# Kernel optimization log

Measured on AMD Instinct MI355X. Metric: run time of the kernel, lower is better.

## Reference

```python
import jax, jax.numpy as jnp
import numpy as np
from jax import lax

C = 64        # channels / number of Phi heads
HID = 8       # Phi hidden size
FEAT = 2 * 8 * 8  # flattened size after conv+pool
EPS = 1e-5
NEG_SLOPE = 0.01


def setup_inputs() -> dict:
    key = jax.random.key(0)
    ks = jax.random.split(key, 12)
    B = 2048
    x1 = jax.random.normal(ks[0], (B, C, 19, 19), dtype=jnp.float32)
    x2 = jax.random.normal(ks[1], (B, C, 19, 19), dtype=jnp.float32)
    s = 0.1
    conv_w = jax.random.normal(ks[2], (C, 2, 2, 3, 3), dtype=jnp.float32) * s
    conv_b = jax.random.normal(ks[3], (C, 2), dtype=jnp.float32) * s
    bn_g = jnp.ones((C, 2), dtype=jnp.float32)
    bn_b = jnp.zeros((C, 2), dtype=jnp.float32)
    fc1_w = jax.random.normal(ks[4], (C, HID, FEAT), dtype=jnp.float32) * s
    fc1_b = jax.random.normal(ks[5], (C, HID), dtype=jnp.float32) * s
    fc2_w = jax.random.normal(ks[6], (C, 1, HID), dtype=jnp.float32) * s
    fc2_b = jax.random.normal(ks[7], (C, 1), dtype=jnp.float32) * s
    w_out = jax.random.normal(ks[8], (1, C), dtype=jnp.float32) * s
    b_out = jax.random.normal(ks[9], (1,), dtype=jnp.float32) * s
    return {
        "x1": x1, "x2": x2,
        "conv_w": conv_w, "conv_b": conv_b,
        "bn_g": bn_g, "bn_b": bn_b,
        "fc1_w": fc1_w, "fc1_b": fc1_b,
        "fc2_w": fc2_w, "fc2_b": fc2_b,
        "w_out": w_out, "b_out": b_out,
    }


def _phi(x, cw, cb, g, b, w1, b1, w2, b2):
    # x: [B,2,19,19], cw: [2,2,3,3]
    y = lax.conv_general_dilated(x, cw, (1, 1), 'VALID',
                                 dimension_numbers=('NCHW', 'OIHW', 'NCHW'))
    y = y + cb[None, :, None, None]                       # [B,2,17,17]
    # BatchNorm2d in training mode: biased batch stats over (N,H,W)
    mean = jnp.mean(y, axis=(0, 2, 3), keepdims=True)
    var = jnp.mean((y - mean) ** 2, axis=(0, 2, 3), keepdims=True)
    y = (y - mean) * lax.rsqrt(var + EPS)
    y = y * g[None, :, None, None] + b[None, :, None, None]
    # LeakyReLU (default slope 0.01)
    y = jnp.where(y > 0, y, NEG_SLOPE * y)
    # MaxPool2d(2): 17x17 -> 8x8 (floor)
    y = lax.reduce_window(y, -jnp.inf, lax.max,
                          (1, 1, 2, 2), (1, 1, 2, 2), 'VALID')
    y = y.reshape(y.shape[0], -1)                         # [B,128]
    y = y @ w1.T + b1                                     # [B,HID]
    y = y @ w2.T + b2                                     # [B,1]
    return y


def reference(x1, x2, conv_w, conv_b, bn_g, bn_b, fc1_w, fc1_b, fc2_w, fc2_b,
              w_out, b_out):
    B = x1.shape[0]
    # per-channel pair input: [C, B, 2, H, W]
    xin = jnp.stack([x1, x2], axis=2).transpose(1, 0, 2, 3, 4)
    outs = jax.vmap(_phi)(xin, conv_w, conv_b, bn_g, bn_b,
                          fc1_w, fc1_b, fc2_w, fc2_b)      # [C, B, 1]
    feat = outs[..., 0].T                                  # [B, C]
    logits = feat @ w_out.T + b_out                        # [B, 1]
    return jax.nn.sigmoid(logits)
```

## Files before the change

kernel.cpp:

```cpp
#include <hip/hip_runtime.h>
#include <math.h>

#define CC    64
#define BATCH 2048
#define EPS   1e-5f
#define SLOPE 0.01f

#define WS_SUMR  0
#define WS_SQR   4096
#define WS_A     8192
#define WS_B     8320
#define WS_WF    8448
#define WS_WB    16640
#define WS_LOGIT 16704
#define WS_POOL  18944
#define WS_NEEDED_BYTES ((size_t)(WS_POOL + (size_t)BATCH * CC * 128) * 4)

__device__ inline unsigned bf16rne(float x) {
    unsigned u = __float_as_uint(x);
    return (u + 0x7fffu + ((u >> 16) & 1u)) >> 16;
}

__device__ inline void pkfma(float2& acc, float2 a, float2 b) {
    asm("v_pk_fma_f32 %0, %1, %2, %0" : "+v"(acc) : "v"(a), "v"(b));
}

template<bool STORE>
__global__ __launch_bounds__(64, 4) void pass1_kernel(
    const float* __restrict__ x1, const float* __restrict__ x2,
    const float* __restrict__ conv_w, const float* __restrict__ conv_b,
    float* __restrict__ ws)
{
    __shared__ __align__(16) float lds[2][760];

    int blk = blockIdx.x;
    int b  = blk >> 5;
    int c0 = (blk & 31) * 2;
    int t  = threadIdx.x;

    const float2* g1 = (const float2*)(x1 + ((size_t)b * 64 + c0) * 361);
    const float2* g2 = (const float2*)(x2 + ((size_t)b * 64 + c0) * 361);
    #pragma unroll
    for (int sl = 0; sl < 6; sl++) {
        int g = t + 64 * sl;
        if (sl < 5 || g < 361) {
            float2 v1 = g1[g];
            float2 v2 = g2[g];
            unsigned e  = 2u * g;
            unsigned r0 = (e * 110377u) >> 21;
            unsigned r1 = ((e + 1u) * 110377u) >> 21;
            int i0 = e + r0;
            int i1 = e + 1 + r1;
            lds[0][i0] = v1.x; lds[0][i1] = v1.y;
            lds[1][i0] = v2.x; lds[1][i1] = v2.y;
        }
    }

    int img = t >> 5;
    int u   = t & 31;
    int o   = u >> 4;
    int p   = u & 15;
    int pi  = p >> 1;
    int pjp = p & 1;
    int c   = c0 + img;

    const float2* wp2 = (const float2*)(conv_w + (size_t)(c * 2 + o) * 18);
    float2 wgt[18];
    #pragma unroll
    for (int j = 0; j < 9; j++) {
        float2 pr = wp2[j];
        wgt[2 * j]     = make_float2(pr.x, pr.x);
        wgt[2 * j + 1] = make_float2(pr.y, pr.y);
    }
    float cbv = conv_b[c * 2 + o];

    __syncthreads();

    float2 A[2][4];
    #pragma unroll
    for (int di = 0; di < 2; di++)
        #pragma unroll
        for (int k = 0; k < 4; k++)
            A[di][k] = make_float2(cbv, cbv);

    int wb = img * 380 + pi * 40 + pjp * 8;

    #pragma unroll
    for (int ic = 0; ic < 2; ic++) {
        const float* plane = &lds[ic][wb];
        const float2* wic = &wgt[ic * 9];
        #pragma unroll
        for (int r = 0; r < 4; r++) {
            const float* row = plane + 20 * r;
            float4 a4 = *(const float4*)(row);
            float4 b4 = *(const float4*)(row + 4);
            float2 c2 = *(const float2*)(row + 8);
            float2 P[9];
            P[0] = make_float2(a4.x, a4.y);
            P[1] = make_float2(a4.y, a4.z);
            P[2] = make_float2(a4.z, a4.w);
            P[3] = make_float2(a4.w, b4.x);
            P[4] = make_float2(b4.x, b4.y);
            P[5] = make_float2(b4.y, b4.z);
            P[6] = make_float2(b4.z, b4.w);
            P[7] = make_float2(b4.w, c2.x);
            P[8] = make_float2(c2.x, c2.y);
            #pragma unroll
            for (int di = 0; di < 2; di++) {
                int ki = r - di;
                if (ki < 0 || ki > 2) continue;
                #pragma unroll
                for (int k = 0; k < 4; k++)
                    #pragma unroll
                    for (int kj = 0; kj < 3; kj++)
                        pkfma(A[di][k], P[2 * k + kj], wic[3 * ki + kj]);
            }
        }
    }

    const float2 one2 = make_float2(1.f, 1.f);
    float2 sp = make_float2(0.f, 0.f), q2 = make_float2(0.f, 0.f);
    #pragma unroll
    for (int di = 0; di < 2; di++)
        #pragma unroll
        for (int k = 0; k < 4; k++) {
            pkfma(sp, A[di][k], one2);
            pkfma(q2, A[di][k], A[di][k]);
        }
    float s = sp.x + sp.y;
    float q = q2.x + q2.y;

    if (STORE) {
        unsigned pk[4];
        #pragma unroll
        for (int k = 0; k < 4; k++) {
            float mx = fmaxf(fmaxf(A[0][k].x, A[0][k].y), fmaxf(A[1][k].x, A[1][k].y));
            float mn = fminf(fminf(A[0][k].x, A[0][k].y), fminf(A[1][k].x, A[1][k].y));
            pk[k] = (bf16rne(mx) << 16) | bf16rne(mn);
        }
        uint4* pool4 = (uint4*)(ws + WS_POOL);
        pool4[((size_t)(b * 64 + c)) * 32 + o * 16 + pi * 2 + pjp] =
            make_uint4(pk[0], pk[1], pk[2], pk[3]);
    }

    int ibase = img * 380;
    #pragma unroll
    for (int rep = 0; rep < 2; rep++) {
        int bidx = p + 16 * rep;
        int bi = bidx < 17 ? 16 : bidx - 17;
        int bj = bidx < 17 ? bidx : 16;
        int bw = ibase + 20 * bi + bj;
        float accb = cbv;
        #pragma unroll
        for (int ic = 0; ic < 2; ic++)
            #pragma unroll
            for (int ki = 0; ki < 3; ki++)
                #pragma unroll
                for (int kj = 0; kj < 3; kj++)
                    accb = fmaf(lds[ic][bw + 20 * ki + kj], wgt[ic * 9 + ki * 3 + kj].x, accb);
        s += accb; q = fmaf(accb, accb, q);
    }
    if (p == 0) {
        int bw = ibase + 20 * 15 + 16;
        float accb = cbv;
        #pragma unroll
        for (int ic = 0; ic < 2; ic++)
            #pragma unroll
            for (int ki = 0; ki < 3; ki++)
                #pragma unroll
                for (int kj = 0; kj < 3; kj++)
                    accb = fmaf(lds[ic][bw + 20 * ki + kj], wgt[ic * 9 + ki * 3 + kj].x, accb);
        s += accb; q = fmaf(accb, accb, q);
    }

    #pragma unroll
    for (int off = 8; off > 0; off >>= 1) {
        s += __shfl_down(s, off, 16);
        q += __shfl_down(q, off, 16);
    }
    if (p == 0) {
        int rep = b & 31;
        atomicAdd(&ws[WS_SUMR + rep * 128 + c * 2 + o], s);
        atomicAdd(&ws[WS_SQR  + rep * 128 + c * 2 + o], q);
    }
}

__global__ __launch_bounds__(128) void prep_kernel(
    const float* __restrict__ bn_g, const float* __restrict__ bn_b,
    const float* __restrict__ fc1_w, const float* __restrict__ fc1_b,
    const float* __restrict__ fc2_w, const float* __restrict__ fc2_b,
    const float* __restrict__ w_out,
    float* __restrict__ ws)
{
    int c = blockIdx.x;
    int f = threadIdx.x;

    float wsum = 0.f;
    #pragma unroll
    for (int h = 0; h < 8; h++)
        wsum += fc2_w[c * 8 + h] * fc1_w[(c * 8 + h) * 128 + f];
    ws[WS_WF + c * 128 + f] = w_out[c] * wsum;

    if (f == 0) {
        float bsum = fc2_b[c];
        #pragma unroll
        for (int h = 0; h < 8; h++)
            bsum += fc2_w[c * 8 + h] * fc1_b[c * 8 + h];
        ws[WS_WB + c] = w_out[c] * bsum;
    }
    if (f < 2) {
        int idx = c * 2 + f;
        float s = 0.f, q = 0.f;
        for (int r = 0; r < 32; r++) {
            s += ws[WS_SUMR + r * 128 + idx];
            q += ws[WS_SQR  + r * 128 + idx];
        }
        const float N = 2048.0f * 289.0f;
        float mean = s / N;
        float var  = q / N - mean * mean;
        float inv  = rsqrtf(var + EPS);
        float A    = bn_g[idx] * inv;
        ws[WS_A + idx] = A;
        ws[WS_B + idx] = bn_b[idx] - mean * A;
    }
}

__global__ __launch_bounds__(256) void pass2_kernel(
    const float* __restrict__ ws, const float* __restrict__ b_out,
    float* __restrict__ out)
{
    __shared__ float red[4];
    int b = blockIdx.x;
    int t = threadIdx.x;
    const uint4* pool = (const uint4*)(ws + WS_POOL) + (size_t)b * 2048;

    float partial = (t < 64) ? ws[WS_WB + t] : 0.f;
    if (t == 0) partial += b_out[0];

    #pragma unroll
    for (int i = 0; i < 8; i++) {
        uint4 p = pool[t + i * 256];
        int k0 = (t + i * 256) * 4;
        float A  = ws[WS_A + (k0 >> 6)];
        float Bs = ws[WS_B + (k0 >> 6)];
        const float4 wf = *(const float4*)&ws[WS_WF + k0];
        unsigned uu[4] = { p.x, p.y, p.z, p.w };
        float wfv[4] = { wf.x, wf.y, wf.z, wf.w };
        #pragma unroll
        for (int j = 0; j < 4; j++) {
            float mx = __uint_as_float(uu[j] & 0xffff0000u);
            float mn = __uint_as_float(uu[j] << 16);
            float val = A > 0.f ? mx : mn;
            float v = fmaf(A, val, Bs);
            v = v > 0.f ? v : SLOPE * v;
            partial = fmaf(v, wfv[j], partial);
        }
    }

    #pragma unroll
    for (int off = 32; off > 0; off >>= 1)
        partial += __shfl_down(partial, off);
    if ((t & 63) == 0) red[t >> 6] = partial;
    __syncthreads();
    if (t == 0) {
        float lsum = red[0] + red[1] + red[2] + red[3];
        out[b] = 1.f / (1.f + expf(-lsum));
    }
}

__global__ __launch_bounds__(128) void main_fb_kernel(
    const float* __restrict__ x1, const float* __restrict__ x2,
    const float* __restrict__ conv_w, const float* __restrict__ conv_b,
    float* __restrict__ ws)
{
    __shared__ float lds[2][19 * 20];
    __shared__ float red[2];

    int blk = blockIdx.x;
    int c = blk & 63;
    int b = blk >> 6;
    int t = threadIdx.x;

    const float* src1 = x1 + (size_t)blk * 361;
    const float* src2 = x2 + (size_t)blk * 361;
    for (int i = t; i < 361; i += 128) {
        int r = i / 19;
        int col = i - r * 19;
        lds[0][r * 20 + col] = src1[i];
        lds[1][r * 20 + col] = src2[i];
    }

    int o = t >> 6;
    int l = t & 63;
    int pi = l >> 3, pj = l & 7;

    const float* wcp = conv_w + c * 36 + o * 18;
    float w0[9], w1[9];
    #pragma unroll
    for (int k = 0; k < 9; k++) { w0[k] = wcp[k]; w1[k] = wcp[9 + k]; }
    float cbv = conv_b[c * 2 + o];
    float A   = ws[WS_A + c * 2 + o];
    float Bs  = ws[WS_B + c * 2 + o];
    float wf  = ws[WS_WF + c * 128 + t];

    __syncthreads();

    float xw[2][4][4];
    int base = (2 * pi) * 20 + 2 * pj;
    #pragma unroll
    for (int ic = 0; ic < 2; ic++)
        #pragma unroll
        for (int r = 0; r < 4; r++)
            #pragma unroll
            for (int cc = 0; cc < 4; cc++)
                xw[ic][r][cc] = lds[ic][base + r * 20 + cc];

    float m = -3.4e38f;
    #pragma unroll
    for (int di = 0; di < 2; di++)
        #pragma unroll
        for (int dj = 0; dj < 2; dj++) {
            float acc = cbv;
            #pragma unroll
            for (int ki = 0; ki < 3; ki++)
                #pragma unroll
                for (int kj = 0; kj < 3; kj++) {
                    acc = fmaf(xw[0][di + ki][dj + kj], w0[ki * 3 + kj], acc);
                    acc = fmaf(xw[1][di + ki][dj + kj], w1[ki * 3 + kj], acc);
                }
            float v = fmaf(A, acc, Bs);
            v = v > 0.f ? v : SLOPE * v;
            m = fmaxf(m, v);
        }

    float contrib = m * wf;
    #pragma unroll
    for (int off = 32; off > 0; off >>= 1)
        contrib += __shfl_down(contrib, off);
    if (l == 0) red[o] = contrib;
    __syncthreads();
    if (t == 0)
        atomicAdd(&ws[WS_LOGIT + b], red[0] + red[1]);
}

__global__ __launch_bounds__(256) void final_fb_kernel(
    const float* __restrict__ ws, const float* __restrict__ b_out,
    float* __restrict__ out)
{
    int b = blockIdx.x * blockDim.x + threadIdx.x;
    if (b >= BATCH) return;
    float bias = b_out[0];
    #pragma unroll
    for (int c = 0; c < CC; c++) bias += ws[WS_WB + c];
    float l = ws[WS_LOGIT + b] + bias;
    out[b] = 1.f / (1.f + expf(-l));
}

extern "C" void kernel_launch(void* const* d_in, const int* in_sizes, int n_in,
                              void* d_out, int out_size, void* d_ws, size_t ws_size,
                              hipStream_t stream) {
    const float* x1     = (const float*)d_in[0];
    const float* x2     = (const float*)d_in[1];
    const float* conv_w = (const float*)d_in[2];
    const float* conv_b = (const float*)d_in[3];
    const float* bn_g   = (const float*)d_in[4];
    const float* bn_b   = (const float*)d_in[5];
    const float* fc1_w  = (const float*)d_in[6];
    const float* fc1_b  = (const float*)d_in[7];
    const float* fc2_w  = (const float*)d_in[8];
    const float* fc2_b  = (const float*)d_in[9];
    const float* w_out  = (const float*)d_in[10];
    const float* b_out  = (const float*)d_in[11];
    float* ws  = (float*)d_ws;
    float* out = (float*)d_out;

    dim3 big(BATCH * 32);
    bool pool_path = ws_size >= WS_NEEDED_BYTES;

    if (pool_path) {
        hipMemsetAsync(d_ws, 0, 8192 * sizeof(float), stream);
        pass1_kernel<true><<<big, 64, 0, stream>>>(x1, x2, conv_w, conv_b, ws);
        prep_kernel<<<CC, 128, 0, stream>>>(bn_g, bn_b, fc1_w, fc1_b, fc2_w, fc2_b, w_out, ws);
        pass2_kernel<<<BATCH, 256, 0, stream>>>(ws, b_out, out);
    } else {
        hipMemsetAsync(d_ws, 0, 18752 * sizeof(float), stream);
        pass1_kernel<false><<<big, 64, 0, stream>>>(x1, x2, conv_w, conv_b, ws);
        prep_kernel<<<CC, 128, 0, stream>>>(bn_g, bn_b, fc1_w, fc1_b, fc2_w, fc2_b, w_out, ws);
        main_fb_kernel<<<dim3(BATCH * CC), 128, 0, stream>>>(x1, x2, conv_w, conv_b, ws);
        final_fb_kernel<<<(BATCH + 255) / 256, 256, 0, stream>>>(ws, b_out, out);
    }
}
```

Measured before the change: 113.3 us.

## Remap pass1 threads to compute both conv outputs per pixel strip in 256-thread blocks

Each thread now computes both output channels for a 2x4 strip of conv outputs, instead of one output channel over a 2x8 strip. This reuses every loaded input row for both filters. Packed FMAs use op_sel to pick weight halves directly, so duplicated weight registers are no longer needed. The kernel also packs four wavefronts (four channel pairs) into 256-thread blocks, each with its own LDS slice, which cuts the block count by four. The edge column and row are recomputed with a new split, including some redundant y16 work on lanes that mask it out. This adds instruction overhead in exchange for input reuse.

```diff
diff --git a/kernel.cpp b/kernel.cpp
--- a/kernel.cpp
+++ b/kernel.cpp
@@ -24,25 +24,38 @@
 __device__ inline void pkfma(float2& acc, float2 a, float2 b) {
     asm("v_pk_fma_f32 %0, %1, %2, %0" : "+v"(acc) : "v"(a), "v"(b));
 }
+__device__ inline void pkfma_l(float2& acc, float2 a, float2 w) {
+    asm("v_pk_fma_f32 %0, %1, %2, %0 op_sel:[0,0,0] op_sel_hi:[1,0,1]"
+        : "+v"(acc) : "v"(a), "v"(w));
+}
+__device__ inline void pkfma_h(float2& acc, float2 a, float2 w) {
+    asm("v_pk_fma_f32 %0, %1, %2, %0 op_sel:[0,1,0] op_sel_hi:[1,1,1]"
+        : "+v"(acc) : "v"(a), "v"(w));
+}
 
 template<bool STORE>
-__global__ __launch_bounds__(64, 4) void pass1_kernel(
+__global__ __launch_bounds__(256, 4) void pass1_kernel(
     const float* __restrict__ x1, const float* __restrict__ x2,
     const float* __restrict__ conv_w, const float* __restrict__ conv_b,
     float* __restrict__ ws)
 {
-    __shared__ __align__(16) float lds[2][760];
+    __shared__ __align__(16) float lds[4][2][760];
 
     int blk = blockIdx.x;
-    int b  = blk >> 5;
-    int c0 = (blk & 31) * 2;
-    int t  = threadIdx.x;
+    int tt  = threadIdx.x;
+    int wv  = tt >> 6;
+    int l   = tt & 63;
+    int b     = blk >> 3;
+    int cpair = (blk & 7) * 4 + wv;
+    int c0    = cpair * 2;
+
+    float (*L)[760] = lds[wv];
 
     const float2* g1 = (const float2*)(x1 + ((size_t)b * 64 + c0) * 361);
     const float2* g2 = (const float2*)(x2 + ((size_t)b * 64 + c0) * 361);
     #pragma unroll
     for (int sl = 0; sl < 6; sl++) {
-        int g = t + 64 * sl;
+        int g = l + 64 * sl;
         if (sl < 5 || g < 361) {
             float2 v1 = g1[g];
             float2 v2 = g2[g];
@@ -51,137 +64,146 @@
             unsigned r1 = ((e + 1u) * 110377u) >> 21;
             int i0 = e + r0;
             int i1 = e + 1 + r1;
-            lds[0][i0] = v1.x; lds[0][i1] = v1.y;
-            lds[1][i0] = v2.x; lds[1][i1] = v2.y;
-        }
-    }
-
-    int img = t >> 5;
-    int u   = t & 31;
-    int o   = u >> 4;
-    int p   = u & 15;
-    int pi  = p >> 1;
-    int pjp = p & 1;
+            L[0][i0] = v1.x; L[0][i1] = v1.y;
+            L[1][i0] = v2.x; L[1][i1] = v2.y;
+        }
+    }
+
+    int img = l >> 5;
+    int u   = l & 31;
+    int pi  = u >> 2;
+    int h   = u & 3;
     int c   = c0 + img;
 
-    const float2* wp2 = (const float2*)(conv_w + (size_t)(c * 2 + o) * 18);
-    float2 wgt[18];
-    #pragma unroll
-    for (int j = 0; j < 9; j++) {
-        float2 pr = wp2[j];
-        wgt[2 * j]     = make_float2(pr.x, pr.x);
-        wgt[2 * j + 1] = make_float2(pr.y, pr.y);
-    }
-    float cbv = conv_b[c * 2 + o];
+    const float2* wpa = (const float2*)(conv_w + (size_t)(c * 2 + 0) * 18);
+    const float2* wpb = (const float2*)(conv_w + (size_t)(c * 2 + 1) * 18);
+    float2 w0[9], w1[9];
+    #pragma unroll
+    for (int j = 0; j < 9; j++) { w0[j] = wpa[j]; w1[j] = wpb[j]; }
+    float cb0 = conv_b[c * 2 + 0];
+    float cb1 = conv_b[c * 2 + 1];
 
     __syncthreads();
 
-    float2 A[2][4];
-    #pragma unroll
-    for (int di = 0; di < 2; di++)
-        #pragma unroll
-        for (int k = 0; k < 4; k++)
-            A[di][k] = make_float2(cbv, cbv);
-
-    int wb = img * 380 + pi * 40 + pjp * 8;
+    float2 A[2][2][2];
+    #pragma unroll
+    for (int cr = 0; cr < 2; cr++)
+        #pragma unroll
+        for (int k = 0; k < 2; k++) {
+            A[0][cr][k] = make_float2(cb0, cb0);
+            A[1][cr][k] = make_float2(cb1, cb1);
+        }
+    float y16[2][2] = { {cb0, cb0}, {cb1, cb1} };
 
     #pragma unroll
     for (int ic = 0; ic < 2; ic++) {
-        const float* plane = &lds[ic][wb];
-        const float2* wic = &wgt[ic * 9];
+        const float* plane = &L[ic][img * 380 + 4 * h];
         #pragma unroll
         for (int r = 0; r < 4; r++) {
-            const float* row = plane + 20 * r;
-            float4 a4 = *(const float4*)(row);
-            float4 b4 = *(const float4*)(row + 4);
-            float2 c2 = *(const float2*)(row + 8);
-            float2 P[9];
-            P[0] = make_float2(a4.x, a4.y);
-            P[1] = make_float2(a4.y, a4.z);
-            P[2] = make_float2(a4.z, a4.w);
-            P[3] = make_float2(a4.w, b4.x);
-            P[4] = make_float2(b4.x, b4.y);
-            P[5] = make_float2(b4.y, b4.z);
-            P[6] = make_float2(b4.z, b4.w);
-            P[7] = make_float2(b4.w, c2.x);
-            P[8] = make_float2(c2.x, c2.y);
+            const float* row = plane + (2 * pi + r) * 20;
+            float4 Xa = *(const float4*)row;
+            float4 Xb = *(const float4*)(row + 4);
+            const float2* Ea = (const float2*)&Xa;
+            const float2* Eb = (const float2*)&Xb;
             #pragma unroll
-            for (int di = 0; di < 2; di++) {
-                int ki = r - di;
+            for (int cr = 0; cr < 2; cr++) {
+                int ki = r - cr;
                 if (ki < 0 || ki > 2) continue;
                 #pragma unroll
-                for (int k = 0; k < 4; k++)
-                    #pragma unroll
-                    for (int kj = 0; kj < 3; kj++)
-                        pkfma(A[di][k], P[2 * k + kj], wic[3 * ki + kj]);
+                for (int o = 0; o < 2; o++) {
+                    const float2* wo = o ? w1 : w0;
+                    const int fb = ic * 9 + ki * 3;
+                    if ((fb & 1) == 0) { pkfma_l(A[o][cr][0], Ea[0], wo[fb >> 1]);
+                                          pkfma_l(A[o][cr][1], Ea[1], wo[fb >> 1]); }
+                    else               { pkfma_h(A[o][cr][0], Ea[0], wo[fb >> 1]);
+                                          pkfma_h(A[o][cr][1], Ea[1], wo[fb >> 1]); }
+                    if (((fb + 2) & 1) == 0) { pkfma_l(A[o][cr][0], Ea[1], wo[(fb + 2) >> 1]);
+                                                pkfma_l(A[o][cr][1], Eb[0], wo[(fb + 2) >> 1]); }
+                    else                      { pkfma_h(A[o][cr][0], Ea[1], wo[(fb + 2) >> 1]);
+                                                pkfma_h(A[o][cr][1], Eb[0], wo[(fb + 2) >> 1]); }
+                    float ws1 = ((fb + 1) & 1) ? wo[(fb + 1) >> 1].y : wo[(fb + 1) >> 1].x;
+                    A[o][cr][0].x = fmaf(Xa.y, ws1, A[o][cr][0].x);
+                    A[o][cr][0].y = fmaf(Xa.z, ws1, A[o][cr][0].y);
+                    A[o][cr][1].x = fmaf(Xa.w, ws1, A[o][cr][1].x);
+                    A[o][cr][1].y = fmaf(Xb.x, ws1, A[o][cr][1].y);
+                    float ws0 = (fb & 1) ? wo[fb >> 1].y : wo[fb >> 1].x;
+                    float ws2 = ((fb + 2) & 1) ? wo[(fb + 2) >> 1].y : wo[(fb + 2) >> 1].x;
+                    y16[o][cr] = fmaf(Xb.x, ws0, y16[o][cr]);
+                    y16[o][cr] = fmaf(Xb.y, ws1, y16[o][cr]);
+                    y16[o][cr] = fmaf(Xb.z, ws2, y16[o][cr]);
+                }
             }
         }
     }
 
     const float2 one2 = make_float2(1.f, 1.f);
-    float2 sp = make_float2(0.f, 0.f), q2 = make_float2(0.f, 0.f);
-    #pragma unroll
-    for (int di = 0; di < 2; di++)
-        #pragma unroll
-        for (int k = 0; k < 4; k++) {
-            pkfma(sp, A[di][k], one2);
-            pkfma(q2, A[di][k], A[di][k]);
-        }
-    float s = sp.x + sp.y;
-    float q = q2.x + q2.y;
-
-    if (STORE) {
-        unsigned pk[4];
-        #pragma unroll
-        for (int k = 0; k < 4; k++) {
-            float mx = fmaxf(fmaxf(A[0][k].x, A[0][k].y), fmaxf(A[1][k].x, A[1][k].y));
-            float mn = fminf(fminf(A[0][k].x, A[0][k].y), fminf(A[1][k].x, A[1][k].y));
-            pk[k] = (bf16rne(mx) << 16) | bf16rne(mn);
-        }
-        uint4* pool4 = (uint4*)(ws + WS_POOL);
-        pool4[((size_t)(b * 64 + c)) * 32 + o * 16 + pi * 2 + pjp] =
-            make_uint4(pk[0], pk[1], pk[2], pk[3]);
-    }
-
-    int ibase = img * 380;
-    #pragma unroll
-    for (int rep = 0; rep < 2; rep++) {
-        int bidx = p + 16 * rep;
-        int bi = bidx < 17 ? 16 : bidx - 17;
-        int bj = bidx < 17 ? bidx : 16;
-        int bw = ibase + 20 * bi + bj;
-        float accb = cbv;
+    float2 SP0 = make_float2(0.f, 0.f), SQ0 = SP0, SP1 = SP0, SQ1 = SP0;
+    #pragma unroll
+    for (int cr = 0; cr < 2; cr++)
+        #pragma unroll
+        for (int k = 0; k < 2; k++) {
+            pkfma(SP0, A[0][cr][k], one2); pkfma(SQ0, A[0][cr][k], A[0][cr][k]);
+            pkfma(SP1, A[1][cr][k], one2); pkfma(SQ1, A[1][cr][k], A[1][cr][k]);
+        }
+    float s0 = SP0.x + SP0.y, q0 = SQ0.x + SQ0.y;
+    float s1 = SP1.x + SP1.y, q1 = SQ1.x + SQ1.y;
+
+    float hm = (h == 3) ? 1.f : 0.f;
+    #pragma unroll
+    for (int cr = 0; cr < 2; cr++) {
+        s0 = fmaf(hm, y16[0][cr], s0); q0 = fmaf(hm * y16[0][cr], y16[0][cr], q0);
+        s1 = fmaf(hm, y16[1][cr], s1); q1 = fmaf(hm * y16[1][cr], y16[1][cr], q1);
+    }
+
+    if (u < 17) {
+        float a0 = cb0, a1 = cb1;
         #pragma unroll
         for (int ic = 0; ic < 2; ic++)
             #pragma unroll
             for (int ki = 0; ki < 3; ki++)
                 #pragma unroll
-                for (int kj = 0; kj < 3; kj++)
-                    accb = fmaf(lds[ic][bw + 20 * ki + kj], wgt[ic * 9 + ki * 3 + kj].x, accb);
-        s += accb; q = fmaf(accb, accb, q);
-    }
-    if (p == 0) {
-        int bw = ibase + 20 * 15 + 16;
-        float accb = cbv;
-        #pragma unroll
-        for (int ic = 0; ic < 2; ic++)
+                for (int kj = 0; kj < 3; kj++) {
+                    float v = L[ic][img * 380 + (16 + ki) * 20 + u + kj];
+                    int ff = ic * 9 + ki * 3 + kj;
+                    float wa = (ff & 1) ? w0[ff >> 1].y : w0[ff >> 1].x;
+                    float wb = (ff & 1) ? w1[ff >> 1].y : w1[ff >> 1].x;
+                    a0 = fmaf(v, wa, a0);
+                    a1 = fmaf(v, wb, a1);
+                }
+        s0 += a0; q0 = fmaf(a0, a0, q0);
+        s1 += a1; q1 = fmaf(a1, a1, q1);
+    }
+
+    if (STORE) {
+        uint2* pool2 = (uint2*)(ws + WS_POOL);
+        #pragma unroll
+        for (int o = 0; o < 2; o++) {
+            unsigned pk[2];
             #pragma unroll
-            for (int ki = 0; ki < 3; ki++)
-                #pragma unroll
-                for (int kj = 0; kj < 3; kj++)
-                    accb = fmaf(lds[ic][bw + 20 * ki + kj], wgt[ic * 9 + ki * 3 + kj].x, accb);
-        s += accb; q = fmaf(accb, accb, q);
-    }
-
-    #pragma unroll
-    for (int off = 8; off > 0; off >>= 1) {
-        s += __shfl_down(s, off, 16);
-        q += __shfl_down(q, off, 16);
-    }
-    if (p == 0) {
+            for (int k = 0; k < 2; k++) {
+                float mx = fmaxf(fmaxf(A[o][0][k].x, A[o][0][k].y),
+                                 fmaxf(A[o][1][k].x, A[o][1][k].y));
+                float mn = fminf(fminf(A[o][0][k].x, A[o][0][k].y),
+                                 fminf(A[o][1][k].x, A[o][1][k].y));
+                pk[k] = (bf16rne(mx) << 16) | bf16rne(mn);
+            }
+            pool2[((size_t)(b * 64 + c)) * 64 + o * 32 + pi * 4 + h] = make_uint2(pk[0], pk[1]);
+        }
+    }
+
+    #pragma unroll
+    for (int off = 16; off > 0; off >>= 1) {
+        s0 += __shfl_down(s0, off, 32);
+        q0 += __shfl_down(q0, off, 32);
+        s1 += __shfl_down(s1, off, 32);
+        q1 += __shfl_down(q1, off, 32);
+    }
+    if (u == 0) {
         int rep = b & 31;
-        atomicAdd(&ws[WS_SUMR + rep * 128 + c * 2 + o], s);
-        atomicAdd(&ws[WS_SQR  + rep * 128 + c * 2 + o], q);
+        atomicAdd(&ws[WS_SUMR + rep * 128 + c * 2 + 0], s0);
+        atomicAdd(&ws[WS_SQR  + rep * 128 + c * 2 + 0], q0);
+        atomicAdd(&ws[WS_SUMR + rep * 128 + c * 2 + 1], s1);
+        atomicAdd(&ws[WS_SQR  + rep * 128 + c * 2 + 1], q1);
     }
 }
 
@@ -374,17 +396,16 @@
     float* ws  = (float*)d_ws;
     float* out = (float*)d_out;
 
-    dim3 big(BATCH * 32);
     bool pool_path = ws_size >= WS_NEEDED_BYTES;
 
     if (pool_path) {
         hipMemsetAsync(d_ws, 0, 8192 * sizeof(float), stream);
-        pass1_kernel<true><<<big, 64, 0, stream>>>(x1, x2, conv_w, conv_b, ws);
+        pass1_kernel<true><<<dim3(BATCH * 8), 256, 0, stream>>>(x1, x2, conv_w, conv_b, ws);
         prep_kernel<<<CC, 128, 0, stream>>>(bn_g, bn_b, fc1_w, fc1_b, fc2_w, fc2_b, w_out, ws);
         pass2_kernel<<<BATCH, 256, 0, stream>>>(ws, b_out, out);
     } else {
         hipMemsetAsync(d_ws, 0, 18752 * sizeof(float), stream);
-        pass1_kernel<false><<<big, 64, 0, stream>>>(x1, x2, conv_w, conv_b, ws);
+        pass1_kernel<false><<<dim3(BATCH * 8), 256, 0, stream>>>(x1, x2, conv_w, conv_b, ws);
         prep_kernel<<<CC, 128, 0, stream>>>(bn_g, bn_b, fc1_w, fc1_b, fc2_w, fc2_b, w_out, ws);
         main_fb_kernel<<<dim3(BATCH * CC), 128, 0, stream>>>(x1, x2, conv_w, conv_b, ws);
         final_fb_kernel<<<(BATCH + 255) / 256, 256, 0, stream>>>(ws, b_out, out);
```

After: 204.4 us. +80.4%, slower.
